# Performance work log

Hardware: AMD Instinct MI355X
Metric: run time of the kernel (lower is better)

Reference implementation:

```python
import jax, jax.numpy as jnp
import numpy as np

S, D, H, DK, DV = 4096, 2048, 16, 128, 128


def setup_inputs() -> dict:
    key = jax.random.key(0)
    ks = jax.random.split(key, 9)
    s = lambda fan_in: 1.0 / np.sqrt(fan_in)
    return {
        "x": jax.random.normal(ks[0], (S, D), dtype=jnp.float32),
        "Wq": jax.random.uniform(ks[1], (H, D, DK), jnp.float32, -s(D), s(D)),
        "bq": jax.random.uniform(ks[2], (H, DK), jnp.float32, -s(D), s(D)),
        "Wk": jax.random.uniform(ks[3], (H, D, DK), jnp.float32, -s(D), s(D)),
        "bk": jax.random.uniform(ks[4], (H, DK), jnp.float32, -s(D), s(D)),
        "Wv": jax.random.uniform(ks[5], (H, D, DV), jnp.float32, -s(D), s(D)),
        "bv": jax.random.uniform(ks[6], (H, DV), jnp.float32, -s(D), s(D)),
        "Wo": jax.random.uniform(ks[7], (H * DV, D), jnp.float32, -s(H * DV), s(H * DV)),
        "bo": jax.random.uniform(ks[8], (D,), jnp.float32, -s(H * DV), s(H * DV)),
    }


def reference(x, Wq, bq, Wk, bk, Wv, bv, Wo, bo):
    # Per-head projections batched over the head axis: [H, S, dk/dv]
    q = jnp.einsum("sd,hdk->hsk", x, Wq) + bq[:, None, :]
    k = jnp.einsum("sd,hdk->hsk", x, Wk) + bk[:, None, :]
    v = jnp.einsum("sd,hdv->hsv", x, Wv) + bv[:, None, :]
    # Scaled dot-product attention per head (mask=None path)
    scores = jnp.einsum("hqk,hsk->hqs", q, k) / jnp.sqrt(jnp.asarray(DK, x.dtype))
    attn = jax.nn.softmax(scores, axis=-1)          # [H, S, S]
    out = jnp.einsum("hqs,hsv->hqv", attn, v)       # [H, S, dv]
    # torch.cat(..., dim=1): interleave heads on feature dim -> [S, H*dv]
    cat = jnp.transpose(out, (1, 0, 2)).reshape(S, H * DV)
    return cat @ Wo + bo
```

## Files before the change

kernel.cpp:

```cpp
#include <hip/hip_runtime.h>
#include <hip/hip_bf16.h>

typedef __attribute__((ext_vector_type(8))) short bhalf8;
typedef __attribute__((ext_vector_type(4))) short bhalf4;
typedef __attribute__((ext_vector_type(4))) float f32x4;
typedef __attribute__((ext_vector_type(16))) float f32x16;
typedef __attribute__((ext_vector_type(4))) unsigned int u32x4;

#define S_SEQ 4096
#define DMODEL 2048
#define NHEAD 16
#define DHEAD 128

__device__ __forceinline__ short f2bf(float f) {
  union { float f; unsigned int u; } v; v.f = f;
  unsigned int r = v.u + 0x7fffu + ((v.u >> 16) & 1u);
  return (short)(r >> 16);
}

__device__ __forceinline__ unsigned pk2(float a, float b) {
  union { __hip_bfloat16 h; unsigned short u; } x, y;
  x.h = __float2bfloat16(a); y.h = __float2bfloat16(b);
  return (unsigned)x.u | ((unsigned)y.u << 16);
}

__global__ __launch_bounds__(256) void k_convert(const float* __restrict__ in,
                                                 short* __restrict__ out, int n4) {
  int i = blockIdx.x * 256 + threadIdx.x;
  if (i >= n4) return;
  f32x4 v = ((const f32x4*)in)[i];
  bhalf4 o;
  o[0] = f2bf(v[0]); o[1] = f2bf(v[1]); o[2] = f2bf(v[2]); o[3] = f2bf(v[3]);
  ((bhalf4*)out)[i] = o;
}

__global__ __launch_bounds__(256) void k_transpose(const float* __restrict__ in,
                                                   short* __restrict__ out, int R, int C) {
  long bs = (long)R * C;
  const float* inp = in + (long)blockIdx.y * bs;
  short* outp = out + (long)blockIdx.y * bs;
  int ct = C >> 6;
  int r0 = (blockIdx.x / ct) << 6;
  int c0 = (blockIdx.x % ct) << 6;
  __shared__ float T[64][65];
  int tid = threadIdx.x;
#pragma unroll
  for (int i = 0; i < 4; i++) {
    int chunk = tid + i * 256;
    int r = chunk >> 4, c = (chunk & 15) << 2;
    f32x4 v = *(const f32x4*)(inp + (long)(r0 + r) * C + c0 + c);
    T[r][c] = v[0]; T[r][c + 1] = v[1]; T[r][c + 2] = v[2]; T[r][c + 3] = v[3];
  }
  __syncthreads();
#pragma unroll
  for (int i = 0; i < 4; i++) {
    int chunk = tid + i * 256;
    int oc = chunk >> 4, o4 = (chunk & 15) << 2;
    bhalf4 o;
    o[0] = f2bf(T[o4][oc]);     o[1] = f2bf(T[o4 + 1][oc]);
    o[2] = f2bf(T[o4 + 2][oc]); o[3] = f2bf(T[o4 + 3][oc]);
    *(bhalf4*)(outp + (long)(c0 + oc) * R + r0 + o4) = o;
  }
}

template <int MODE>
__global__ __launch_bounds__(256) void k_gemm(const short* __restrict__ A, int lda, long a_bs,
                                              const short* __restrict__ Bt, int ldb, long b_bs,
                                              void* __restrict__ Cp, int ldc, long c_bs,
                                              const float* __restrict__ bias, int bias_bs,
                                              float alpha,
                                              int Mtiles, int Ntiles, int K) {
  const int b = blockIdx.y;
  A += (long)b * a_bs;
  Bt += (long)b * b_bs;
  bias += (long)b * bias_bs;
  const int bx = blockIdx.x;
  const int mt = bx / Ntiles, nt = bx % Ntiles;
  const int row0 = mt << 7, col0 = nt << 7;
  const int tid = threadIdx.x;
  const int wave = tid >> 6, lane = tid & 63;
  const int wr = wave >> 1, wc = wave & 1;
  const int lr = lane & 15, lg = lane >> 4;

  __shared__ short As[128][72];
  __shared__ short Bs[128][72];

  f32x4 acc[4][4];
#pragma unroll
  for (int mi = 0; mi < 4; mi++)
#pragma unroll
    for (int ni = 0; ni < 4; ni++) acc[mi][ni] = (f32x4){0.f, 0.f, 0.f, 0.f};

  for (int k0 = 0; k0 < K; k0 += 64) {
    __syncthreads();
#pragma unroll
    for (int i = 0; i < 4; i++) {
      int chunk = tid + i * 256;
      int r = chunk >> 3, c = (chunk & 7) << 3;
      *(bhalf8*)&As[r][c] = *(const bhalf8*)(A + (long)(row0 + r) * lda + k0 + c);
      *(bhalf8*)&Bs[r][c] = *(const bhalf8*)(Bt + (long)(col0 + r) * ldb + k0 + c);
    }
    __syncthreads();
#pragma unroll
    for (int kk = 0; kk < 2; kk++) {
      bhalf8 af[4], bf[4];
#pragma unroll
      for (int mi = 0; mi < 4; mi++)
        af[mi] = *(const bhalf8*)&As[wr * 64 + mi * 16 + lr][kk * 32 + lg * 8];
#pragma unroll
      for (int ni = 0; ni < 4; ni++)
        bf[ni] = *(const bhalf8*)&Bs[wc * 64 + ni * 16 + lr][kk * 32 + lg * 8];
#pragma unroll
      for (int mi = 0; mi < 4; mi++)
#pragma unroll
        for (int ni = 0; ni < 4; ni++)
          acc[mi][ni] = __builtin_amdgcn_mfma_f32_16x16x32_bf16(af[mi], bf[ni], acc[mi][ni], 0, 0, 0);
    }
  }

#pragma unroll
  for (int mi = 0; mi < 4; mi++) {
#pragma unroll
    for (int ni = 0; ni < 4; ni++) {
#pragma unroll
      for (int r = 0; r < 4; r++) {
        int row = row0 + wr * 64 + mi * 16 + lg * 4 + r;
        int col = col0 + wc * 64 + ni * 16 + lr;
        float v = acc[mi][ni][r];
        if (MODE == 0) {
          v = (v + bias[col]) * alpha;
          ((short*)Cp)[(long)b * c_bs + (long)row * ldc + col] = f2bf(v);
        } else if (MODE == 1) {
          v = (v + bias[row]) * alpha;
          ((short*)Cp)[(long)b * c_bs + (long)row * ldc + col] = f2bf(v);
        } else {
          v += bias[col];
          ((float*)Cp)[(long)b * c_bs + (long)row * ldc + col] = v;
        }
      }
    }
  }
}

__global__ __launch_bounds__(256, 2) void k_attn(const short* __restrict__ q,
                                                 const short* __restrict__ k,
                                                 const short* __restrict__ vT,
                                                 short* __restrict__ cat) {
  __shared__ __align__(16) char smem[65536];
  const int wg = blockIdx.x;
  const int wgid = (wg & 7) * 64 + (wg >> 3);
  const int h = wgid >> 5;
  const int q0 = (wgid & 31) << 7;
  const int tid = threadIdx.x;
  const int wave = tid >> 6;
  const int l31 = tid & 31;
  const int hi = (tid >> 5) & 1;
  const int swl = (tid & 15) << 4;

  const long qk_base = (long)h * S_SEQ * DHEAD;
  const long vt_base = (long)h * DHEAD * S_SEQ;

  {
    u32x4 qst[8];
#pragma unroll
    for (int rnd = 0; rnd < 8; rnd++) {
      int o = rnd * 4096 + tid * 16;
      int row = o >> 8, col = o & 255;
      qst[rnd] = *(const u32x4*)(q + qk_base + (long)(q0 + row) * DHEAD + (col >> 1));
    }
#pragma unroll
    for (int rnd = 0; rnd < 8; rnd++) {
      int o = rnd * 4096 + tid * 16;
      int row = o >> 8, col = o & 255;
      *(u32x4*)(smem + row * 256 + (col ^ ((row & 15) << 4))) = qst[rnd];
    }
  }
  __syncthreads();
  bhalf8 qf[8];
#pragma unroll
  for (int kc = 0; kc < 8; kc++) {
    int row = wave * 32 + l31;
    qf[kc] = *(const bhalf8*)(smem + row * 256 + ((kc * 32 + hi * 16) ^ swl));
  }
  __syncthreads();

  f32x16 accO[4];
#pragma unroll
  for (int d = 0; d < 4; d++)
#pragma unroll
    for (int r = 0; r < 16; r++) accO[d][r] = 0.f;
  float m_run = -1e30f, l_part = 0.f;

  u32x4 st[8];
  auto load_tile = [&](int kv0) {
#pragma unroll
    for (int rnd = 0; rnd < 4; rnd++) {
      int o = rnd * 4096 + tid * 16;
      int row = o >> 8, col = o & 255;
      st[rnd] = *(const u32x4*)(k + qk_base + (long)(kv0 + row) * DHEAD + (col >> 1));
    }
#pragma unroll
    for (int rnd = 0; rnd < 4; rnd++) {
      int o = rnd * 4096 + tid * 16;
      int dv = o >> 7, col = o & 127;
      st[4 + rnd] = *(const u32x4*)(vT + vt_base + (long)dv * S_SEQ + kv0 + (col >> 1));
    }
  };
  auto write_tile = [&](char* buf) {
#pragma unroll
    for (int rnd = 0; rnd < 4; rnd++) {
      int o = rnd * 4096 + tid * 16;
      int row = o >> 8, col = o & 255;
      *(u32x4*)(buf + row * 256 + (col ^ ((row & 15) << 4))) = st[rnd];
    }
#pragma unroll
    for (int rnd = 0; rnd < 4; rnd++) {
      int o = rnd * 4096 + tid * 16;
      int dv = o >> 7, col = o & 127;
      *(u32x4*)(buf + 16384 + (dv & 63) * 256 +
                ((((dv >> 6) << 7) + col) ^ ((dv & 15) << 4))) = st[4 + rnd];
    }
  };

  load_tile(0);
  write_tile(smem);
  load_tile(64);
  __syncthreads();

  const int NT = S_SEQ / 64;
  for (int t = 0; t < NT; t++) {
    char* buf = smem + (t & 1) * 32768;

    f32x16 accS[2];
#pragma unroll
    for (int kvb = 0; kvb < 2; kvb++)
#pragma unroll
      for (int r = 0; r < 16; r++) accS[kvb][r] = 0.f;

    __builtin_amdgcn_s_setprio(1);
#pragma unroll
    for (int kvb = 0; kvb < 2; kvb++) {
      int row = kvb * 32 + l31;
#pragma unroll
      for (int kc = 0; kc < 8; kc++) {
        bhalf8 kf = *(const bhalf8*)(buf + row * 256 + ((kc * 32 + hi * 16) ^ swl));
        accS[kvb] = __builtin_amdgcn_mfma_f32_32x32x16_bf16(kf, qf[kc], accS[kvb], 0, 0, 0);
      }
    }
    __builtin_amdgcn_s_setprio(0);

    float mx[8];
#pragma unroll
    for (int g = 0; g < 8; g++) {
      const int kvb = g >> 2, b4 = (g & 3) * 4;
      mx[g] = fmaxf(fmaxf(accS[kvb][b4], accS[kvb][b4 + 1]),
                    fmaxf(accS[kvb][b4 + 2], accS[kvb][b4 + 3]));
    }
    float mc = fmaxf(fmaxf(fmaxf(mx[0], mx[1]), fmaxf(mx[2], mx[3])),
                     fmaxf(fmaxf(mx[4], mx[5]), fmaxf(mx[6], mx[7])));
    mc = fmaxf(mc, __shfl_xor(mc, 32));

    if (!__all(mc <= m_run + 8.f)) {
      float mn = fmaxf(m_run, mc);
      float corr = __builtin_amdgcn_exp2f(m_run - mn);
      m_run = mn;
      l_part *= corr;
#pragma unroll
      for (int d = 0; d < 4; d++)
#pragma unroll
        for (int r = 0; r < 16; r++) accO[d][r] *= corr;
    }

    unsigned pk[2][4][2];
#pragma unroll
    for (int kvb = 0; kvb < 2; kvb++)
#pragma unroll
      for (int g = 0; g < 4; g++) {
        float p0 = __builtin_amdgcn_exp2f(accS[kvb][4 * g + 0] - m_run);
        float p1 = __builtin_amdgcn_exp2f(accS[kvb][4 * g + 1] - m_run);
        float p2 = __builtin_amdgcn_exp2f(accS[kvb][4 * g + 2] - m_run);
        float p3 = __builtin_amdgcn_exp2f(accS[kvb][4 * g + 3] - m_run);
        l_part += (p0 + p1) + (p2 + p3);
        pk[kvb][g][0] = pk2(p0, p1);
        pk[kvb][g][1] = pk2(p2, p3);
      }

    bhalf8 pa[4];
#pragma unroll
    for (int kvb = 0; kvb < 2; kvb++)
#pragma unroll
      for (int c1 = 0; c1 < 2; c1++) {
        unsigned a0 = pk[kvb][2 * c1][0],     a1 = pk[kvb][2 * c1][1];
        unsigned b0 = pk[kvb][2 * c1 + 1][0], b1 = pk[kvb][2 * c1 + 1][1];
        unsigned s0a = (unsigned)__shfl_xor((int)a0, 32);
        unsigned s1a = (unsigned)__shfl_xor((int)a1, 32);
        unsigned s0b = (unsigned)__shfl_xor((int)b0, 32);
        unsigned s1b = (unsigned)__shfl_xor((int)b1, 32);
        union { unsigned u[4]; bhalf8 v; } cvt;
        cvt.u[0] = hi ? s0b : a0;
        cvt.u[1] = hi ? s1b : a1;
        cvt.u[2] = hi ? b0 : s0a;
        cvt.u[3] = hi ? b1 : s1a;
        pa[kvb * 2 + c1] = cvt.v;
      }

    __builtin_amdgcn_s_setprio(1);
#pragma unroll
    for (int d = 0; d < 4; d++) {
      int vrow = ((d & 1) << 5) + l31;
      int vhalf = (d >> 1) << 7;
#pragma unroll
      for (int c = 0; c < 4; c++) {
        bhalf8 vf = *(const bhalf8*)(buf + 16384 + vrow * 256 +
                                     ((vhalf + c * 32 + hi * 16) ^ swl));
        accO[d] = __builtin_amdgcn_mfma_f32_32x32x16_bf16(vf, pa[c], accO[d], 0, 0, 0);
      }
    }
    __builtin_amdgcn_s_setprio(0);

    if (t + 1 < NT) write_tile(smem + ((t + 1) & 1) * 32768);
    __syncthreads();
    if (t + 2 < NT) load_tile((t + 2) * 64);
  }

  float l_tot = l_part + __shfl_xor(l_part, 32);
  float inv = 1.f / l_tot;
  long rowbase = (long)(q0 + wave * 32 + l31) * DMODEL + h * DHEAD;
#pragma unroll
  for (int d = 0; d < 4; d++)
#pragma unroll
    for (int rg = 0; rg < 4; rg++) {
      bhalf4 ov;
#pragma unroll
      for (int i = 0; i < 4; i++) ov[i] = f2bf(accO[d][rg * 4 + i] * inv);
      *(bhalf4*)(cat + rowbase + d * 32 + rg * 8 + hi * 4) = ov;
    }
}

extern "C" void kernel_launch(void* const* d_in, const int* in_sizes, int n_in,
                              void* d_out, int out_size, void* d_ws, size_t ws_size,
                              hipStream_t stream) {
  const float* x  = (const float*)d_in[0];
  const float* Wq = (const float*)d_in[1];
  const float* bq = (const float*)d_in[2];
  const float* Wk = (const float*)d_in[3];
  const float* bk = (const float*)d_in[4];
  const float* Wv = (const float*)d_in[5];
  const float* bv = (const float*)d_in[6];
  const float* Wo = (const float*)d_in[7];
  const float* bo = (const float*)d_in[8];
  float* out = (float*)d_out;

  short* x_bf   = (short*)d_ws;
  short* Wqt    = x_bf  + (long)S_SEQ * DMODEL;
  short* Wkt    = Wqt   + (long)NHEAD * DHEAD * DMODEL;
  short* Wvt    = Wkt   + (long)NHEAD * DHEAD * DMODEL;
  short* Wot    = Wvt   + (long)NHEAD * DHEAD * DMODEL;
  short* q_bf   = Wot   + (long)DMODEL * DMODEL;
  short* k_bf   = q_bf  + (long)NHEAD * S_SEQ * DHEAD;
  short* vT_bf  = k_bf  + (long)NHEAD * S_SEQ * DHEAD;
  short* cat_bf = vT_bf + (long)NHEAD * DHEAD * S_SEQ;

  dim3 blk(256);

  k_convert<<<dim3((S_SEQ * DMODEL / 4 + 255) / 256), blk, 0, stream>>>(x, x_bf, S_SEQ * DMODEL / 4);

  k_transpose<<<dim3((DMODEL / 64) * (DHEAD / 64), NHEAD), blk, 0, stream>>>(Wq, Wqt, DMODEL, DHEAD);
  k_transpose<<<dim3((DMODEL / 64) * (DHEAD / 64), NHEAD), blk, 0, stream>>>(Wk, Wkt, DMODEL, DHEAD);
  k_transpose<<<dim3((DMODEL / 64) * (DHEAD / 64), NHEAD), blk, 0, stream>>>(Wv, Wvt, DMODEL, DHEAD);
  k_transpose<<<dim3((DMODEL / 64) * (DMODEL / 64), 1), blk, 0, stream>>>(Wo, Wot, DMODEL, DMODEL);

  const float alpha_q = 0.08838834764831845f * 1.4426950408889634f;

  k_gemm<0><<<dim3(32, NHEAD), blk, 0, stream>>>(x_bf, DMODEL, 0L,
                                                 Wqt, DMODEL, (long)DHEAD * DMODEL,
                                                 q_bf, DHEAD, (long)S_SEQ * DHEAD,
                                                 bq, DHEAD, alpha_q, 32, 1, DMODEL);
  k_gemm<0><<<dim3(32, NHEAD), blk, 0, stream>>>(x_bf, DMODEL, 0L,
                                                 Wkt, DMODEL, (long)DHEAD * DMODEL,
                                                 k_bf, DHEAD, (long)S_SEQ * DHEAD,
                                                 bk, DHEAD, 1.0f, 32, 1, DMODEL);
  k_gemm<1><<<dim3(32, NHEAD), blk, 0, stream>>>(Wvt, DMODEL, (long)DHEAD * DMODEL,
                                                 x_bf, DMODEL, 0L,
                                                 vT_bf, S_SEQ, (long)DHEAD * S_SEQ,
                                                 bv, DHEAD, 1.0f, 1, 32, DMODEL);

  k_attn<<<dim3(512), blk, 0, stream>>>(q_bf, k_bf, vT_bf, cat_bf);

  k_gemm<2><<<dim3(32 * 16, 1), blk, 0, stream>>>(cat_bf, DMODEL, 0L,
                                                  Wot, DMODEL, 0L,
                                                  out, DMODEL, 0L,
                                                  bo, 0, 1.0f, 32, 16, DMODEL);
}
```

Baseline: 375.4 us.

## Split attention KV range in two with partial outputs and merge kernel

```diff
diff --git a/kernel.cpp b/kernel.cpp
--- a/kernel.cpp
+++ b/kernel.cpp
@@ -17,7 +17,10 @@
   unsigned int r = v.u + 0x7fffu + ((v.u >> 16) & 1u);
   return (short)(r >> 16);
 }
-
+__device__ __forceinline__ float bf2f(short s) {
+  union { unsigned int u; float f; } v; v.u = ((unsigned int)(unsigned short)s) << 16;
+  return v.f;
+}
 __device__ __forceinline__ unsigned pk2(float a, float b) {
   union { __hip_bfloat16 h; unsigned short u; } x, y;
   x.h = __float2bfloat16(a); y.h = __float2bfloat16(b);
@@ -142,15 +145,19 @@
   }
 }
 
-__global__ __launch_bounds__(256, 2) void k_attn(const short* __restrict__ q,
+__global__ __launch_bounds__(256, 4) void k_attn(const short* __restrict__ q,
                                                  const short* __restrict__ k,
                                                  const short* __restrict__ vT,
-                                                 short* __restrict__ cat) {
-  __shared__ __align__(16) char smem[65536];
+                                                 short* __restrict__ Opart,
+                                                 float* __restrict__ mlbuf) {
+  __shared__ __align__(16) char smem[32768];
   const int wg = blockIdx.x;
-  const int wgid = (wg & 7) * 64 + (wg >> 3);
-  const int h = wgid >> 5;
-  const int q0 = (wgid & 31) << 7;
+  const int wgid = (wg & 7) * 128 + (wg >> 3);
+  const int h = wgid >> 6;
+  const int qt = (wgid & 63) >> 1;
+  const int half = wgid & 1;
+  const int q0 = qt << 7;
+  const int kvbase = half << 11;
   const int tid = threadIdx.x;
   const int wave = tid >> 6;
   const int l31 = tid & 31;
@@ -191,73 +198,65 @@
     for (int r = 0; r < 16; r++) accO[d][r] = 0.f;
   float m_run = -1e30f, l_part = 0.f;
 
-  u32x4 st[8];
+  u32x4 st[4];
   auto load_tile = [&](int kv0) {
 #pragma unroll
-    for (int rnd = 0; rnd < 4; rnd++) {
+    for (int rnd = 0; rnd < 2; rnd++) {
       int o = rnd * 4096 + tid * 16;
       int row = o >> 8, col = o & 255;
       st[rnd] = *(const u32x4*)(k + qk_base + (long)(kv0 + row) * DHEAD + (col >> 1));
     }
 #pragma unroll
-    for (int rnd = 0; rnd < 4; rnd++) {
-      int o = rnd * 4096 + tid * 16;
-      int dv = o >> 7, col = o & 127;
-      st[4 + rnd] = *(const u32x4*)(vT + vt_base + (long)dv * S_SEQ + kv0 + (col >> 1));
+    for (int rnd = 0; rnd < 2; rnd++) {
+      int o = rnd * 4096 + tid * 16;
+      int dv = o >> 6, col = o & 63;
+      st[2 + rnd] = *(const u32x4*)(vT + vt_base + (long)dv * S_SEQ + kv0 + (col >> 1));
     }
   };
   auto write_tile = [&](char* buf) {
 #pragma unroll
-    for (int rnd = 0; rnd < 4; rnd++) {
+    for (int rnd = 0; rnd < 2; rnd++) {
       int o = rnd * 4096 + tid * 16;
       int row = o >> 8, col = o & 255;
       *(u32x4*)(buf + row * 256 + (col ^ ((row & 15) << 4))) = st[rnd];
     }
 #pragma unroll
-    for (int rnd = 0; rnd < 4; rnd++) {
-      int o = rnd * 4096 + tid * 16;
-      int dv = o >> 7, col = o & 127;
-      *(u32x4*)(buf + 16384 + (dv & 63) * 256 +
-                ((((dv >> 6) << 7) + col) ^ ((dv & 15) << 4))) = st[4 + rnd];
+    for (int rnd = 0; rnd < 2; rnd++) {
+      int o = rnd * 4096 + tid * 16;
+      int dv = o >> 6, col = o & 63;
+      *(u32x4*)(buf + 8192 + (dv & 31) * 256 +
+                ((((dv >> 5) << 6) | col) ^ ((dv & 15) << 4))) = st[2 + rnd];
     }
   };
 
-  load_tile(0);
+  load_tile(kvbase);
   write_tile(smem);
-  load_tile(64);
+  load_tile(kvbase + 32);
   __syncthreads();
 
-  const int NT = S_SEQ / 64;
+  const int NT = 2048 / 32;
   for (int t = 0; t < NT; t++) {
-    char* buf = smem + (t & 1) * 32768;
-
-    f32x16 accS[2];
-#pragma unroll
-    for (int kvb = 0; kvb < 2; kvb++)
-#pragma unroll
-      for (int r = 0; r < 16; r++) accS[kvb][r] = 0.f;
+    char* buf = smem + (t & 1) * 16384;
+
+    f32x16 accS;
+#pragma unroll
+    for (int r = 0; r < 16; r++) accS[r] = 0.f;
 
     __builtin_amdgcn_s_setprio(1);
 #pragma unroll
-    for (int kvb = 0; kvb < 2; kvb++) {
-      int row = kvb * 32 + l31;
-#pragma unroll
-      for (int kc = 0; kc < 8; kc++) {
-        bhalf8 kf = *(const bhalf8*)(buf + row * 256 + ((kc * 32 + hi * 16) ^ swl));
-        accS[kvb] = __builtin_amdgcn_mfma_f32_32x32x16_bf16(kf, qf[kc], accS[kvb], 0, 0, 0);
-      }
+    for (int kc = 0; kc < 8; kc++) {
+      bhalf8 kf = *(const bhalf8*)(buf + l31 * 256 + ((kc * 32 + hi * 16) ^ swl));
+      accS = __builtin_amdgcn_mfma_f32_32x32x16_bf16(kf, qf[kc], accS, 0, 0, 0);
     }
     __builtin_amdgcn_s_setprio(0);
 
-    float mx[8];
-#pragma unroll
-    for (int g = 0; g < 8; g++) {
-      const int kvb = g >> 2, b4 = (g & 3) * 4;
-      mx[g] = fmaxf(fmaxf(accS[kvb][b4], accS[kvb][b4 + 1]),
-                    fmaxf(accS[kvb][b4 + 2], accS[kvb][b4 + 3]));
-    }
-    float mc = fmaxf(fmaxf(fmaxf(mx[0], mx[1]), fmaxf(mx[2], mx[3])),
-                     fmaxf(fmaxf(mx[4], mx[5]), fmaxf(mx[6], mx[7])));
+    float mx[4];
+#pragma unroll
+    for (int g = 0; g < 4; g++) {
+      int b4 = g * 4;
+      mx[g] = fmaxf(fmaxf(accS[b4], accS[b4 + 1]), fmaxf(accS[b4 + 2], accS[b4 + 3]));
+    }
+    float mc = fmaxf(fmaxf(mx[0], mx[1]), fmaxf(mx[2], mx[3]));
     mc = fmaxf(mc, __shfl_xor(mc, 32));
 
     if (!__all(mc <= m_run + 8.f)) {
@@ -271,70 +270,106 @@
         for (int r = 0; r < 16; r++) accO[d][r] *= corr;
     }
 
-    unsigned pk[2][4][2];
-#pragma unroll
-    for (int kvb = 0; kvb < 2; kvb++)
-#pragma unroll
-      for (int g = 0; g < 4; g++) {
-        float p0 = __builtin_amdgcn_exp2f(accS[kvb][4 * g + 0] - m_run);
-        float p1 = __builtin_amdgcn_exp2f(accS[kvb][4 * g + 1] - m_run);
-        float p2 = __builtin_amdgcn_exp2f(accS[kvb][4 * g + 2] - m_run);
-        float p3 = __builtin_amdgcn_exp2f(accS[kvb][4 * g + 3] - m_run);
-        l_part += (p0 + p1) + (p2 + p3);
-        pk[kvb][g][0] = pk2(p0, p1);
-        pk[kvb][g][1] = pk2(p2, p3);
-      }
-
-    bhalf8 pa[4];
-#pragma unroll
-    for (int kvb = 0; kvb < 2; kvb++)
-#pragma unroll
-      for (int c1 = 0; c1 < 2; c1++) {
-        unsigned a0 = pk[kvb][2 * c1][0],     a1 = pk[kvb][2 * c1][1];
-        unsigned b0 = pk[kvb][2 * c1 + 1][0], b1 = pk[kvb][2 * c1 + 1][1];
-        unsigned s0a = (unsigned)__shfl_xor((int)a0, 32);
-        unsigned s1a = (unsigned)__shfl_xor((int)a1, 32);
-        unsigned s0b = (unsigned)__shfl_xor((int)b0, 32);
-        unsigned s1b = (unsigned)__shfl_xor((int)b1, 32);
-        union { unsigned u[4]; bhalf8 v; } cvt;
-        cvt.u[0] = hi ? s0b : a0;
-        cvt.u[1] = hi ? s1b : a1;
-        cvt.u[2] = hi ? b0 : s0a;
-        cvt.u[3] = hi ? b1 : s1a;
-        pa[kvb * 2 + c1] = cvt.v;
-      }
+    unsigned pk[4][2];
+#pragma unroll
+    for (int g = 0; g < 4; g++) {
+      float p0 = __builtin_amdgcn_exp2f(accS[4 * g + 0] - m_run);
+      float p1 = __builtin_amdgcn_exp2f(accS[4 * g + 1] - m_run);
+      float p2 = __builtin_amdgcn_exp2f(accS[4 * g + 2] - m_run);
+      float p3 = __builtin_amdgcn_exp2f(accS[4 * g + 3] - m_run);
+      l_part += (p0 + p1) + (p2 + p3);
+      pk[g][0] = pk2(p0, p1);
+      pk[g][1] = pk2(p2, p3);
+    }
+
+    bhalf8 pa[2];
+#pragma unroll
+    for (int c1 = 0; c1 < 2; c1++) {
+      unsigned a0 = pk[2 * c1][0],     a1 = pk[2 * c1][1];
+      unsigned b0 = pk[2 * c1 + 1][0], b1 = pk[2 * c1 + 1][1];
+      unsigned s0a = (unsigned)__shfl_xor((int)a0, 32);
+      unsigned s1a = (unsigned)__shfl_xor((int)a1, 32);
+      unsigned s0b = (unsigned)__shfl_xor((int)b0, 32);
+      unsigned s1b = (unsigned)__shfl_xor((int)b1, 32);
+      union { unsigned u[4]; bhalf8 v; } cvt;
+      cvt.u[0] = hi ? s0b : a0;
+      cvt.u[1] = hi ? s1b : a1;
+      cvt.u[2] = hi ? b0 : s0a;
+      cvt.u[3] = hi ? b1 : s1a;
+      pa[c1] = cvt.v;
+    }
 
     __builtin_amdgcn_s_setprio(1);
 #pragma unroll
     for (int d = 0; d < 4; d++) {
-      int vrow = ((d & 1) << 5) + l31;
-      int vhalf = (d >> 1) << 7;
-#pragma unroll
-      for (int c = 0; c < 4; c++) {
-        bhalf8 vf = *(const bhalf8*)(buf + 16384 + vrow * 256 +
-                                     ((vhalf + c * 32 + hi * 16) ^ swl));
+#pragma unroll
+      for (int c = 0; c < 2; c++) {
+        bhalf8 vf = *(const bhalf8*)(buf + 8192 + l31 * 256 +
+                                     (((d << 6) | (c * 32 + hi * 16)) ^ swl));
         accO[d] = __builtin_amdgcn_mfma_f32_32x32x16_bf16(vf, pa[c], accO[d], 0, 0, 0);
       }
     }
     __builtin_amdgcn_s_setprio(0);
 
-    if (t + 1 < NT) write_tile(smem + ((t + 1) & 1) * 32768);
+    if (t + 1 < NT) write_tile(smem + ((t + 1) & 1) * 16384);
     __syncthreads();
-    if (t + 2 < NT) load_tile((t + 2) * 64);
+    if (t + 2 < NT) load_tile(kvbase + (t + 2) * 32);
   }
 
   float l_tot = l_part + __shfl_xor(l_part, 32);
-  float inv = 1.f / l_tot;
-  long rowbase = (long)(q0 + wave * 32 + l31) * DMODEL + h * DHEAD;
+  const int pidx = wgid;
+  const int qloc = wave * 32 + l31;
+  long obase = (long)pidx * 16384 + (long)qloc * 128;
 #pragma unroll
   for (int d = 0; d < 4; d++)
 #pragma unroll
     for (int rg = 0; rg < 4; rg++) {
       bhalf4 ov;
 #pragma unroll
-      for (int i = 0; i < 4; i++) ov[i] = f2bf(accO[d][rg * 4 + i] * inv);
-      *(bhalf4*)(cat + rowbase + d * 32 + rg * 8 + hi * 4) = ov;
-    }
+      for (int i = 0; i < 4; i++) ov[i] = f2bf(accO[d][rg * 4 + i]);
+      *(bhalf4*)(Opart + obase + d * 32 + rg * 8 + hi * 4) = ov;
+    }
+  if (hi == 0) {
+    mlbuf[(long)pidx * 256 + qloc] = m_run;
+    mlbuf[(long)pidx * 256 + 128 + qloc] = l_tot;
+  }
+}
+
+__global__ __launch_bounds__(256) void k_merge(const short* __restrict__ Opart,
+                                               const float* __restrict__ mlbuf,
+                                               short* __restrict__ cat) {
+  const int b = blockIdx.x;
+  const int h = b >> 5, qt = b & 31;
+  const int p0 = h * 64 + qt * 2;
+  __shared__ float w1[128], w2[128];
+  const int t = threadIdx.x;
+  if (t < 128) {
+    float m1 = mlbuf[(long)p0 * 256 + t];
+    float l1 = mlbuf[(long)p0 * 256 + 128 + t];
+    float m2 = mlbuf[(long)(p0 + 1) * 256 + t];
+    float l2 = mlbuf[(long)(p0 + 1) * 256 + 128 + t];
+    float m = fmaxf(m1, m2);
+    float e1 = __builtin_amdgcn_exp2f(m1 - m);
+    float e2 = __builtin_amdgcn_exp2f(m2 - m);
+    float inv = 1.f / (e1 * l1 + e2 * l2);
+    w1[t] = e1 * inv;
+    w2[t] = e2 * inv;
+  }
+  __syncthreads();
+  const int qq = t >> 1, d0 = (t & 1) * 64;
+  const short* o1 = Opart + (long)p0 * 16384 + (long)qq * 128 + d0;
+  const short* o2 = o1 + 16384;
+  short* dst = cat + (long)(qt * 128 + qq) * DMODEL + h * DHEAD + d0;
+  const float a = w1[qq], c = w2[qq];
+#pragma unroll
+  for (int i = 0; i < 8; i++) {
+    bhalf8 x = *(const bhalf8*)(o1 + i * 8);
+    bhalf8 y = *(const bhalf8*)(o2 + i * 8);
+    bhalf8 o;
+#pragma unroll
+    for (int j = 0; j < 8; j++) o[j] = f2bf(bf2f(x[j]) * a + bf2f(y[j]) * c);
+    *(bhalf8*)(dst + i * 8) = o;
+  }
 }
 
 extern "C" void kernel_launch(void* const* d_in, const int* in_sizes, int n_in,
@@ -361,6 +396,9 @@
   short* vT_bf  = k_bf  + (long)NHEAD * S_SEQ * DHEAD;
   short* cat_bf = vT_bf + (long)NHEAD * DHEAD * S_SEQ;
 
+  short* Opart  = x_bf;
+  float* mlbuf  = (float*)(Opart + (long)1024 * 16384);
+
   dim3 blk(256);
 
   k_convert<<<dim3((S_SEQ * DMODEL / 4 + 255) / 256), blk, 0, stream>>>(x, x_bf, S_SEQ * DMODEL / 4);
@@ -385,7 +423,8 @@
                                                  vT_bf, S_SEQ, (long)DHEAD * S_SEQ,
                                                  bv, DHEAD, 1.0f, 1, 32, DMODEL);
 
-  k_attn<<<dim3(512), blk, 0, stream>>>(q_bf, k_bf, vT_bf, cat_bf);
+  k_attn<<<dim3(1024), blk, 0, stream>>>(q_bf, k_bf, vT_bf, Opart, mlbuf);
+  k_merge<<<dim3(512), blk, 0, stream>>>(Opart, mlbuf, cat_bf);
 
   k_gemm<2><<<dim3(32 * 16, 1), blk, 0, stream>>>(cat_bf, DMODEL, 0L,
                                                   Wot, DMODEL, 0L,
```

After: 686.1 us. +82.8%, slower.
